# Optimization experiments

Hardware: AMD Instinct MI355X
Metric: run time of the kernel (lower is better)

Reference implementation:

```python
import jax, jax.numpy as jnp
import numpy as np

BINS = 5
POINTS = 2
EPS_DIV = 1e-6
GN_GROUPS = 32
GN_EPS = 1e-5


def bilinear_sum(img, ys, xs):
    """Sum of bilinear samples with zero padding outside the image.
    img: (B, C, H, W); ys, xs: (B, K, H, W) absolute sample coords.
    Returns (B, C, H, W) = sum over K of bilinear(img, ys_k, xs_k)."""
    B, C, H, W = img.shape
    K = ys.shape[1]
    y0 = jnp.floor(ys)
    x0 = jnp.floor(xs)
    imgf = img.reshape(B, C, H * W)
    acc = jnp.zeros((B, C, K, H, W), img.dtype)
    for dy, dx in ((0, 0), (0, 1), (1, 0), (1, 1)):
        yi = y0 + dy
        xi = x0 + dx
        w = (1.0 - jnp.abs(ys - yi)) * (1.0 - jnp.abs(xs - xi))
        valid = (yi >= 0) & (yi <= H - 1) & (xi >= 0) & (xi <= W - 1)
        yc = jnp.clip(yi, 0, H - 1).astype(jnp.int32)
        xc = jnp.clip(xi, 0, W - 1).astype(jnp.int32)
        idx = (yc * W + xc).reshape(B, 1, K * H * W)
        g = jnp.take_along_axis(imgf, idx, axis=2).reshape(B, C, K, H, W)
        acc = acc + (w * valid.astype(img.dtype))[:, None] * g
    return acc.sum(axis=2)


def setup_inputs():
    key = jax.random.key(0)
    ks = jax.random.split(key, 6)
    B, C, H, W = 2, 256, 100, 152
    P, K = POINTS, BINS
    x = jax.random.normal(ks[0], (B, C, H, W), jnp.float32)
    offsets = jax.random.normal(ks[1], (B, P * K * 2, H, W), jnp.float32) * 2.0
    ef_w = jax.random.normal(ks[2], (P * C, C), jnp.float32) * 0.02
    ef_b = jnp.zeros((P * C,), jnp.float32)
    hm1_w = jax.random.normal(ks[3], (P, C, C), jnp.float32) * 0.02
    hm1_b = jnp.zeros((P, C), jnp.float32)
    hm2_w = jax.random.normal(ks[4], (P, C), jnp.float32) * 0.02
    hm2_b = jnp.zeros((P,), jnp.float32)
    merge_w = jax.random.normal(ks[5], (C, P * C), jnp.float32) * 0.02
    merge_b = jnp.zeros((C,), jnp.float32)
    gn_g = jnp.ones((C,), jnp.float32)
    gn_b = jnp.zeros((C,), jnp.float32)
    return {"x": x, "offsets": offsets, "ef_w": ef_w, "ef_b": ef_b,
            "hm1_w": hm1_w, "hm1_b": hm1_b, "hm2_w": hm2_w, "hm2_b": hm2_b,
            "merge_w": merge_w, "merge_b": merge_b, "gn_g": gn_g, "gn_b": gn_b}


def reference(x, offsets, ef_w, ef_b, hm1_w, hm1_b, hm2_w, hm2_b, merge_w, merge_b, gn_g, gn_b):
    B, C, H, W = x.shape
    P, K = POINTS, BINS
    # expand_feat: 1x1 conv C -> P*C
    ef = jnp.einsum('bchw,dc->bdhw', x, ef_w) + ef_b[None, :, None, None]
    efp = ef.reshape(B, P, C, H, W)
    # heatmap: grouped 1x1 conv (per-point) -> ReLU -> grouped 1x1 conv -> exp
    h = jax.nn.relu(jnp.einsum('bpchw,pdc->bpdhw', efp, hm1_w) + hm1_b[None, :, :, None, None])
    heat = jnp.exp(jnp.einsum('bpdhw,pd->bphw', h, hm2_w) + hm2_b[None, :, None, None])  # (B,P,H,W)
    # offsets: (B, P, K, 2, H, W) with channel layout [y, x] per bin.
    # base_offset cancels the [1,bins] kernel grid, so the deform conv with
    # all-ones weights is simply: sum over bins of bilinear samples at
    # (h + off_y, w + off_x).
    off = offsets.reshape(B, P, K, 2, H, W)
    hg = jnp.arange(H, dtype=x.dtype)[None, None, None, :, None]
    wg = jnp.arange(W, dtype=x.dtype)[None, None, None, None, :]
    ys = hg + off[:, :, :, 0]  # (B,P,K,H,W)
    xs = wg + off[:, :, :, 1]
    outs = []
    for p in range(P):
        # sample feat*heat (C channels) and heat (1 channel) together
        img = jnp.concatenate([efp[:, p] * heat[:, p][:, None], heat[:, p][:, None]], axis=1)
        s = bilinear_sum(img, ys[:, p], xs[:, p])  # (B, C+1, H, W)
        outs.append(s[:, :C] / (s[:, C:] + EPS_DIV))
    outs = jnp.concatenate(outs, axis=1)  # (B, P*C, H, W)
    merged = jnp.einsum('bchw,dc->bdhw', outs, merge_w) + merge_b[None, :, None, None]
    # GroupNorm(32, C) + ReLU
    g = merged.reshape(B, GN_GROUPS, C // GN_GROUPS, H, W)
    mu = g.mean(axis=(2, 3, 4), keepdims=True)
    var = g.var(axis=(2, 3, 4), keepdims=True)
    gn = ((g - mu) / jnp.sqrt(var + GN_EPS)).reshape(B, C, H, W)
    gn = gn * gn_g[None, :, None, None] + gn_b[None, :, None, None]
    return jax.nn.relu(gn)
```

## Files before the change

### kernel.cpp

```cpp
#include <hip/hip_runtime.h>

#define BINS 5
#define PTS  2
constexpr int Bx = 2, Cc = 256, Hh = 100, Ww = 152;
constexpr int HW = Hh * Ww;
constexpr int NTILE = 238;
constexpr float EPS_DIV = 1e-6f;
constexpr float GN_EPS  = 1e-5f;

typedef __attribute__((ext_vector_type(8))) short bfrag;
typedef __attribute__((ext_vector_type(4))) float f32x4;

__device__ __forceinline__ ushort f2bf(float f) {
    union { float f; unsigned u; } v; v.f = f;
    unsigned r = v.u + 0x7fffu + ((v.u >> 16) & 1u);
    return (ushort)(r >> 16);
}
__device__ __forceinline__ float bflo(unsigned u) {
    return __uint_as_float(u << 16);
}
__device__ __forceinline__ float bfhi(unsigned u) {
    return __uint_as_float(u & 0xffff0000u);
}
__device__ __forceinline__ unsigned pack2(float a, float b) {
    return (unsigned)f2bf(a) | ((unsigned)f2bf(b) << 16);
}

__global__ __launch_bounds__(256)
void k_wconv(const float* __restrict__ efw, const float* __restrict__ w1,
             const float* __restrict__ mw, ushort* __restrict__ wb)
{
    int gid = blockIdx.x * 256 + threadIdx.x;
    int e = gid * 4;
    int arr = e >> 17, off = e & 131071;
    const float* src = arr == 0 ? efw : (arr == 1 ? w1 : mw);
    float4 v = *(const float4*)(src + off);
    ushort4 o = { f2bf(v.x), f2bf(v.y), f2bf(v.z), f2bf(v.w) };
    *(ushort4*)(wb + e) = o;
}

__global__ __launch_bounds__(256)
void k_xt(const float* __restrict__ x, ushort* __restrict__ xbt)
{
    __shared__ float tile[32][33];
    const int t = threadIdx.x;
    const int hw0 = blockIdx.x * 32;
    const int c0 = blockIdx.y * 32;
    const int b = blockIdx.z;
    const float* xb = x + ((size_t)b * Cc + c0) * HW + hw0;
    const int tx = t & 31, ty = t >> 5;
    #pragma unroll
    for (int r = 0; r < 4; r++) {
        int c = ty + r * 8;
        tile[c][tx] = xb[(size_t)c * HW + tx];
    }
    __syncthreads();
    const int hwl = t >> 3, c4 = (t & 7) * 4;
    ushort4 o = { f2bf(tile[c4 + 0][hwl]), f2bf(tile[c4 + 1][hwl]),
                  f2bf(tile[c4 + 2][hwl]), f2bf(tile[c4 + 3][hwl]) };
    *(ushort4*)&xbt[((size_t)b * HW + hw0 + hwl) * Cc + c0 + c4] = o;
}

__global__ __launch_bounds__(256)
void k_ef(const ushort* __restrict__ xbt, const ushort* __restrict__ wbe,
          const float* __restrict__ efb, ushort* __restrict__ efp)
{
    __shared__ ushort As[128 * 72];
    __shared__ ushort Bs[64 * 72];
    const int t = threadIdx.x;
    const int wv = t >> 6, ln = t & 63;
    const int quad = ln >> 4, l16 = ln & 15;
    const int pix0 = blockIdx.x * 64;
    const int n0 = blockIdx.y * 128;
    const int b = blockIdx.z;
    const ushort* xb = xbt + (size_t)b * HW * Cc;

    f32x4 acc[2][4];
    #pragma unroll
    for (int i = 0; i < 2; i++)
        #pragma unroll
        for (int j = 0; j < 4; j++) acc[i][j] = (f32x4){0.f, 0.f, 0.f, 0.f};

    const int arow = t >> 3, acol = (t & 7) * 8;
    const int srow = t >> 3, scol = (t & 7) * 8;

    for (int k0 = 0; k0 < 256; k0 += 64) {
        #pragma unroll
        for (int r = 0; r < 4; r++) {
            int row = arow + r * 32;
            *(uint4*)&As[row * 72 + acol] =
                *(const uint4*)&wbe[(size_t)(n0 + row) * 256 + k0 + acol];
        }
        #pragma unroll
        for (int r = 0; r < 2; r++) {
            int row = srow + r * 32;
            int pq = pix0 + row; if (pq > HW - 1) pq = HW - 1;
            *(uint4*)&Bs[row * 72 + scol] =
                *(const uint4*)&xb[(size_t)pq * Cc + k0 + scol];
        }
        __syncthreads();
        #pragma unroll
        for (int kk = 0; kk < 64; kk += 32) {
            bfrag af[2], bfr[4];
            #pragma unroll
            for (int dt = 0; dt < 2; dt++)
                af[dt] = *(const bfrag*)&As[(wv * 32 + dt * 16 + l16) * 72 + kk + quad * 8];
            #pragma unroll
            for (int pt = 0; pt < 4; pt++)
                bfr[pt] = *(const bfrag*)&Bs[(pt * 16 + l16) * 72 + kk + quad * 8];
            #pragma unroll
            for (int dt = 0; dt < 2; dt++)
                #pragma unroll
                for (int pt = 0; pt < 4; pt++)
                    acc[dt][pt] = __builtin_amdgcn_mfma_f32_16x16x32_bf16(
                        af[dt], bfr[pt], acc[dt][pt], 0, 0, 0);
        }
        __syncthreads();
    }

    float bias[2][4];
    #pragma unroll
    for (int dt = 0; dt < 2; dt++)
        #pragma unroll
        for (int r = 0; r < 4; r++)
            bias[dt][r] = efb[n0 + wv * 32 + dt * 16 + quad * 4 + r];
    #pragma unroll
    for (int dt = 0; dt < 2; dt++)
        #pragma unroll
        for (int pt = 0; pt < 4; pt++) {
            int pix = pt * 16 + l16;
            int ch = wv * 32 + dt * 16 + quad * 4;
            ushort4 o = { f2bf(acc[dt][pt][0] + bias[dt][0]),
                          f2bf(acc[dt][pt][1] + bias[dt][1]),
                          f2bf(acc[dt][pt][2] + bias[dt][2]),
                          f2bf(acc[dt][pt][3] + bias[dt][3]) };
            *(ushort4*)&As[pix * 136 + ch] = o;
        }
    __syncthreads();
    const int p = n0 >> 8, cbase = n0 & 255;
    ushort* outb = efp + (size_t)((b * PTS + p) * HW) * Cc;
    #pragma unroll
    for (int r = 0; r < 4; r++) {
        int pix = (t >> 4) + r * 16;
        int ch8 = (t & 15) * 8;
        if (pix0 + pix < HW)
            *(uint4*)&outb[(size_t)(pix0 + pix) * Cc + cbase + ch8] =
                *(const uint4*)&As[pix * 136 + ch8];
    }
}

__global__ __launch_bounds__(256)
void k_heat(const ushort* __restrict__ efp, const ushort* __restrict__ wb1,
            const float* __restrict__ b1, const float* __restrict__ w2,
            const float* __restrict__ b2, float* __restrict__ heat)
{
    __shared__ ushort As[256 * 72];
    __shared__ ushort Bs[64 * 72];
    __shared__ float red[4][64];
    const int t = threadIdx.x;
    const int wv = t >> 6, ln = t & 63;
    const int quad = ln >> 4, l16 = ln & 15;
    const int pix0 = blockIdx.x * 64;
    const int p = blockIdx.y;
    const int b = blockIdx.z;
    const ushort* efb_ = efp + (size_t)((b * PTS + p) * HW) * Cc;
    const ushort* w1p = wb1 + (size_t)p * Cc * Cc;

    f32x4 acc[4][4];
    #pragma unroll
    for (int i = 0; i < 4; i++)
        #pragma unroll
        for (int j = 0; j < 4; j++) acc[i][j] = (f32x4){0.f, 0.f, 0.f, 0.f};

    const int srow = t >> 3, scol = (t & 7) * 8;

    for (int k0 = 0; k0 < 256; k0 += 64) {
        #pragma unroll
        for (int r = 0; r < 8; r++) {
            int row = srow + r * 32;
            *(uint4*)&As[row * 72 + scol] =
                *(const uint4*)&w1p[(size_t)row * 256 + k0 + scol];
        }
        #pragma unroll
        for (int r = 0; r < 2; r++) {
            int row = srow + r * 32;
            int pq = pix0 + row; if (pq > HW - 1) pq = HW - 1;
            *(uint4*)&Bs[row * 72 + scol] =
                *(const uint4*)&efb_[(size_t)pq * Cc + k0 + scol];
        }
        __syncthreads();
        #pragma unroll
        for (int kk = 0; kk < 64; kk += 32) {
            bfrag af[4], bfr[4];
            #pragma unroll
            for (int dt = 0; dt < 4; dt++)
                af[dt] = *(const bfrag*)&As[(wv * 64 + dt * 16 + l16) * 72 + kk + quad * 8];
            #pragma unroll
            for (int pt = 0; pt < 4; pt++)
                bfr[pt] = *(const bfrag*)&Bs[(pt * 16 + l16) * 72 + kk + quad * 8];
            #pragma unroll
            for (int dt = 0; dt < 4; dt++)
                #pragma unroll
                for (int pt = 0; pt < 4; pt++)
                    acc[dt][pt] = __builtin_amdgcn_mfma_f32_16x16x32_bf16(
                        af[dt], bfr[pt], acc[dt][pt], 0, 0, 0);
        }
        __syncthreads();
    }

    const float* b1p = b1 + p * 256;
    const float* w2p = w2 + p * 256;
    float s[4] = {0.f, 0.f, 0.f, 0.f};
    #pragma unroll
    for (int dt = 0; dt < 4; dt++) {
        int chb = wv * 64 + dt * 16 + quad * 4;
        float bb[4], ww[4];
        #pragma unroll
        for (int r = 0; r < 4; r++) { bb[r] = b1p[chb + r]; ww[r] = w2p[chb + r]; }
        #pragma unroll
        for (int pt = 0; pt < 4; pt++)
            #pragma unroll
            for (int r = 0; r < 4; r++) {
                float h = acc[dt][pt][r] + bb[r];
                h = h > 0.f ? h : 0.f;
                s[pt] += ww[r] * h;
            }
    }
    #pragma unroll
    for (int pt = 0; pt < 4; pt++) {
        s[pt] += __shfl_xor(s[pt], 16);
        s[pt] += __shfl_xor(s[pt], 32);
    }
    if (ln < 16) {
        #pragma unroll
        for (int pt = 0; pt < 4; pt++) red[wv][pt * 16 + ln] = s[pt];
    }
    __syncthreads();
    if (t < 64) {
        float v = red[0][t] + red[1][t] + red[2][t] + red[3][t] + b2[p];
        int m = pix0 + t;
        if (m < HW) heat[(size_t)(b * PTS + p) * HW + m] = expf(v);
    }
}

__global__ __launch_bounds__(256)
void k_sample(const ushort* __restrict__ efp, const float* __restrict__ heat,
              const float* __restrict__ offs, ushort* __restrict__ outs)
{
    __shared__ uint2 s_wo[32][20];
    const int t = threadIdx.x;
    const int bid = blockIdx.x;
    const int nx = (bid & 7) * 60 + (bid >> 3);
    if (nx >= 475) return;
    const int m0 = nx * 32;
    const int p = blockIdx.y;
    const int b = blockIdx.z;
    const float* heat_bp = heat + (size_t)(b * PTS + p) * HW;

    if (t < 32 * BINS) {
        int j = t / BINS, k = t % BINS;
        int hw = m0 + j;
        int hh = hw / Ww, ww = hw % Ww;
        int chy = (p * BINS + k) * 2;
        float oy = offs[((size_t)b * (PTS * BINS * 2) + chy)     * HW + hw];
        float ox = offs[((size_t)b * (PTS * BINS * 2) + chy + 1) * HW + hw];
        float ysf = (float)hh + oy;
        float xsf = (float)ww + ox;
        float y0 = floorf(ysf), x0 = floorf(xsf);
        #pragma unroll
        for (int dy = 0; dy < 2; dy++)
            #pragma unroll
            for (int dx = 0; dx < 2; dx++) {
                float yi = y0 + dy, xi = x0 + dx;
                float wgt = (1.f - fabsf(ysf - yi)) * (1.f - fabsf(xsf - xi));
                bool valid = (yi >= 0.f) && (yi <= (float)(Hh - 1)) &&
                             (xi >= 0.f) && (xi <= (float)(Ww - 1));
                int yc = (int)yi; yc = yc < 0 ? 0 : (yc > Hh - 1 ? Hh - 1 : yc);
                int xc = (int)xi; xc = xc < 0 ? 0 : (xc > Ww - 1 ? Ww - 1 : xc);
                int idx = yc * Ww + xc;
                float wh = valid ? wgt * heat_bp[idx] : 0.f;
                s_wo[j][k * 4 + dy * 2 + dx] =
                    make_uint2(__float_as_uint(wh), (unsigned)idx << 9);
            }
    }
    __syncthreads();
    if (t < 32) {
        float s = 0.f;
        #pragma unroll
        for (int u = 0; u < 20; u++) s += __uint_as_float(s_wo[t][u].x);
        float inv = 1.f / (s + EPS_DIV);
        #pragma unroll
        for (int u = 0; u < 20; u++)
            s_wo[t][u].x = __float_as_uint(__uint_as_float(s_wo[t][u].x) * inv);
    }
    __syncthreads();

    const int wv = t >> 6, ln = t & 63;
    const int half = ln >> 5, c8 = ln & 31;
    const char* efbase = (const char*)(efp + (size_t)((b * PTS + p) * HW) * Cc)
                         + c8 * 16;
    ushort* ob = outs + ((size_t)(b * HW + m0)) * (PTS * Cc) + p * Cc + c8 * 8;
    #pragma unroll
    for (int i = 0; i < 8; i += 2) {
        const int j = wv * 8 + i + half;
        float a[8] = {0.f, 0.f, 0.f, 0.f, 0.f, 0.f, 0.f, 0.f};
        #pragma unroll
        for (int u = 0; u < 20; u++) {
            uint2 wo = s_wo[j][u];
            uint4 v = *(const uint4*)(efbase + wo.y);
            float w = __uint_as_float(wo.x);
            a[0] += w * bflo(v.x); a[1] += w * bfhi(v.x);
            a[2] += w * bflo(v.y); a[3] += w * bfhi(v.y);
            a[4] += w * bflo(v.z); a[5] += w * bfhi(v.z);
            a[6] += w * bflo(v.w); a[7] += w * bfhi(v.w);
        }
        uint4 o = { pack2(a[0], a[1]), pack2(a[2], a[3]),
                    pack2(a[4], a[5]), pack2(a[6], a[7]) };
        *(uint4*)(ob + (size_t)j * (PTS * Cc)) = o;
    }
}

__global__ __launch_bounds__(256)
void k_merge(const ushort* __restrict__ outs, const ushort* __restrict__ wbm,
             const float* __restrict__ mb, ushort* __restrict__ mgb,
             float* __restrict__ part2)
{
    __shared__ ushort As[64 * 72];
    __shared__ ushort Bs[64 * 72];
    const int t = threadIdx.x;
    const int wv = t >> 6, ln = t & 63;
    const int quad = ln >> 4, l16 = ln & 15;
    const int pix0 = blockIdx.x * 64;
    const int n0 = blockIdx.y * 64;
    const int b = blockIdx.z;
    const ushort* ob = outs + (size_t)b * HW * (PTS * Cc);

    f32x4 acc[4];
    #pragma unroll
    for (int j = 0; j < 4; j++) acc[j] = (f32x4){0.f, 0.f, 0.f, 0.f};

    const int srow = t >> 3, scol = (t & 7) * 8;

    for (int k0 = 0; k0 < 512; k0 += 64) {
        #pragma unroll
        for (int r = 0; r < 2; r++) {
            int row = srow + r * 32;
            *(uint4*)&As[row * 72 + scol] =
                *(const uint4*)&wbm[(size_t)(n0 + row) * 512 + k0 + scol];
        }
        #pragma unroll
        for (int r = 0; r < 2; r++) {
            int row = srow + r * 32;
            int pq = pix0 + row; if (pq > HW - 1) pq = HW - 1;
            *(uint4*)&Bs[row * 72 + scol] =
                *(const uint4*)&ob[(size_t)pq * (PTS * Cc) + k0 + scol];
        }
        __syncthreads();
        #pragma unroll
        for (int kk = 0; kk < 64; kk += 32) {
            bfrag af = *(const bfrag*)&As[(wv * 16 + l16) * 72 + kk + quad * 8];
            #pragma unroll
            for (int pt = 0; pt < 4; pt++) {
                bfrag bfr = *(const bfrag*)&Bs[(pt * 16 + l16) * 72 + kk + quad * 8];
                acc[pt] = __builtin_amdgcn_mfma_f32_16x16x32_bf16(
                    af, bfr, acc[pt], 0, 0, 0);
            }
        }
        __syncthreads();
    }

    const int ch = n0 + wv * 16 + quad * 4;
    float bias[4];
    #pragma unroll
    for (int r = 0; r < 4; r++) bias[r] = mb[ch + r];

    float sacc = 0.f, qacc = 0.f;
    #pragma unroll
    for (int pt = 0; pt < 4; pt++) {
        int pix = pix0 + pt * 16 + l16;
        if (pix < HW) {
            #pragma unroll
            for (int r = 0; r < 4; r++) {
                float v = acc[pt][r] + bias[r];
                mgb[((size_t)b * Cc + ch + r) * HW + pix] = f2bf(v);
                sacc += v; qacc += v * v;
            }
        }
    }
    #pragma unroll
    for (int off = 1; off <= 16; off <<= 1) {
        sacc += __shfl_xor(sacc, off);
        qacc += __shfl_xor(qacc, off);
    }
    if ((ln & 31) == 0) {
        int g = (n0 >> 3) + wv * 2 + (quad >> 1);
        size_t idx = ((size_t)(b * 32 + g) * NTILE + blockIdx.x) * 2;
        part2[idx + 0] = sacc;
        part2[idx + 1] = qacc;
    }
}

__global__ __launch_bounds__(256)
void k_gnfinal(const float* __restrict__ part2, float* __restrict__ statf)
{
    const int bg = blockIdx.x;
    const int t = threadIdx.x;
    float s = 0.f, q = 0.f;
    if (t < NTILE) {
        s = part2[((size_t)bg * NTILE + t) * 2 + 0];
        q = part2[((size_t)bg * NTILE + t) * 2 + 1];
    }
    #pragma unroll
    for (int off = 1; off <= 32; off <<= 1) {
        s += __shfl_xor(s, off);
        q += __shfl_xor(q, off);
    }
    __shared__ float rs[4], rq[4];
    int wid = t >> 6;
    if ((t & 63) == 0) { rs[wid] = s; rq[wid] = q; }
    __syncthreads();
    if (t == 0) {
        float S = rs[0] + rs[1] + rs[2] + rs[3];
        float Q = rq[0] + rq[1] + rq[2] + rq[3];
        const float n = 8.f * HW;
        float mean = S / n;
        float var  = Q / n - mean * mean;
        statf[bg * 2 + 0] = mean;
        statf[bg * 2 + 1] = rsqrtf(var + GN_EPS);
    }
}

__global__ __launch_bounds__(256)
void k_gnapply(const ushort* __restrict__ mgb, const float* __restrict__ statf,
               const float* __restrict__ gg, const float* __restrict__ gb,
               float* __restrict__ out)
{
    const int i8 = blockIdx.x * 256 + threadIdx.x;
    const int i = i8 * 8;
    const int CHW = Cc * HW;
    const int b = i / CHW;
    const int r = i - b * CHW;
    const int c = r / HW;
    const int g = c >> 3;
    float mean = statf[(b * 32 + g) * 2 + 0];
    float istd = statf[(b * 32 + g) * 2 + 1];
    float sc = istd * gg[c];
    float sh = gb[c] - mean * sc;
    uint4 v = *(const uint4*)(mgb + i);
    float4 o0, o1;
    o0.x = fmaxf(bflo(v.x) * sc + sh, 0.f);
    o0.y = fmaxf(bfhi(v.x) * sc + sh, 0.f);
    o0.z = fmaxf(bflo(v.y) * sc + sh, 0.f);
    o0.w = fmaxf(bfhi(v.y) * sc + sh, 0.f);
    o1.x = fmaxf(bflo(v.z) * sc + sh, 0.f);
    o1.y = fmaxf(bfhi(v.z) * sc + sh, 0.f);
    o1.z = fmaxf(bflo(v.w) * sc + sh, 0.f);
    o1.w = fmaxf(bfhi(v.w) * sc + sh, 0.f);
    *(float4*)(out + i)     = o0;
    *(float4*)(out + i + 4) = o1;
}

extern "C" void kernel_launch(void* const* d_in, const int* in_sizes, int n_in,
                              void* d_out, int out_size, void* d_ws, size_t ws_size,
                              hipStream_t stream)
{
    const float* x    = (const float*)d_in[0];
    const float* offs = (const float*)d_in[1];
    const float* efw  = (const float*)d_in[2];
    const float* efb  = (const float*)d_in[3];
    const float* w1   = (const float*)d_in[4];
    const float* b1   = (const float*)d_in[5];
    const float* w2   = (const float*)d_in[6];
    const float* b2   = (const float*)d_in[7];
    const float* mw   = (const float*)d_in[8];
    const float* mb   = (const float*)d_in[9];
    const float* gg   = (const float*)d_in[10];
    const float* gb   = (const float*)d_in[11];
    float* out = (float*)d_out;

    ushort* wb    = (ushort*)d_ws;
    ushort* wbe   = wb;
    ushort* wb1   = wb + 131072;
    ushort* wbm   = wb + 262144;
    ushort* efp   = wb + 393216;
    ushort* outsb = efp + (size_t)Bx * PTS * HW * Cc;
    ushort* xbt   = outsb + (size_t)Bx * HW * PTS * Cc;
    ushort* mgb   = xbt + (size_t)Bx * HW * Cc;
    float*  heat  = (float*)(mgb + (size_t)Bx * Cc * HW);
    float*  part2 = heat + (size_t)Bx * PTS * HW;
    float*  statf = part2 + (size_t)64 * NTILE * 2;

    dim3 blk(256);
    k_wconv  <<<dim3(384),              blk, 0, stream>>>(efw, w1, mw, wb);
    k_xt     <<<dim3(475, 8, Bx),       blk, 0, stream>>>(x, xbt);
    k_ef     <<<dim3(238, 4, Bx),       blk, 0, stream>>>(xbt, wbe, efb, efp);
    k_heat   <<<dim3(238, PTS, Bx),     blk, 0, stream>>>(efp, wb1, b1, w2, b2, heat);
    k_sample <<<dim3(480, PTS, Bx),     blk, 0, stream>>>(efp, heat, offs, outsb);
    k_merge  <<<dim3(NTILE, 4, Bx),     blk, 0, stream>>>(outsb, wbm, mb, mgb, part2);
    k_gnfinal<<<dim3(64),               blk, 0, stream>>>(part2, statf);
    k_gnapply<<<dim3(Bx * Cc * HW / 8 / 256), blk, 0, stream>>>(mgb, statf, gg, gb, out);
}
```

Baseline: 212.3 us.

## Fold expand-conv weights into heat and merge GEMMs, sample raw x directly

Uses the linearity of the 1x1 expand conv to remove the k_ef GEMM and the efp intermediate. The expand weights are pre-multiplied into the heat-MLP first layer and into the merge weights, and bilinear sampling now reads the transposed bf16 x. The expand bias is carried as a per-pixel term: the normalized heat-weight sum is saved to sbuf and multiplied by a folded bias vector in the merge epilogue. This drops a large GEMM and its memory traffic, but adds a small fp32 weight-combination kernel each call and changes bf16 rounding points.

```diff
diff --git a/kernel.cpp b/kernel.cpp
--- a/kernel.cpp
+++ b/kernel.cpp
@@ -27,19 +27,6 @@
 }
 
 __global__ __launch_bounds__(256)
-void k_wconv(const float* __restrict__ efw, const float* __restrict__ w1,
-             const float* __restrict__ mw, ushort* __restrict__ wb)
-{
-    int gid = blockIdx.x * 256 + threadIdx.x;
-    int e = gid * 4;
-    int arr = e >> 17, off = e & 131071;
-    const float* src = arr == 0 ? efw : (arr == 1 ? w1 : mw);
-    float4 v = *(const float4*)(src + off);
-    ushort4 o = { f2bf(v.x), f2bf(v.y), f2bf(v.z), f2bf(v.w) };
-    *(ushort4*)(wb + e) = o;
-}
-
-__global__ __launch_bounds__(256)
 void k_xt(const float* __restrict__ x, ushort* __restrict__ xbt)
 {
     __shared__ float tile[32][33];
@@ -62,34 +49,96 @@
 }
 
 __global__ __launch_bounds__(256)
-void k_ef(const ushort* __restrict__ xbt, const ushort* __restrict__ wbe,
-          const float* __restrict__ efb, ushort* __restrict__ efp)
-{
-    __shared__ ushort As[128 * 72];
+void k_wcomb(const float* __restrict__ efw, const float* __restrict__ w1,
+             const float* __restrict__ mw, ushort* __restrict__ whb,
+             ushort* __restrict__ cmb)
+{
+    __shared__ float Wt[16][256];
+    const int t = threadIdx.x;
+    const int tile = blockIdx.x, p = blockIdx.y, which = blockIdx.z;
+    if (which == 0) {
+        const float* src = w1 + (size_t)p * 65536 + (size_t)tile * 16 * 256;
+        #pragma unroll
+        for (int i = 0; i < 16; i++) Wt[i][t] = src[i * 256 + t];
+    } else {
+        #pragma unroll
+        for (int i = 0; i < 16; i++)
+            Wt[i][t] = mw[((size_t)(tile * 16 + i)) * 512 + p * 256 + t];
+    }
+    __syncthreads();
+    float acc[16];
+    #pragma unroll
+    for (int r = 0; r < 16; r++) acc[r] = 0.f;
+    const float* eb = efw + (size_t)p * 256 * 256;
+    for (int d = 0; d < 256; d++) {
+        float v = eb[(size_t)d * 256 + t];
+        #pragma unroll
+        for (int r = 0; r < 16; r++) acc[r] += Wt[r][d] * v;
+    }
+    if (which == 0) {
+        #pragma unroll
+        for (int r = 0; r < 16; r++)
+            whb[(size_t)p * 65536 + (size_t)(tile * 16 + r) * 256 + t] = f2bf(acc[r]);
+    } else {
+        #pragma unroll
+        for (int r = 0; r < 16; r++)
+            cmb[(size_t)(tile * 16 + r) * 512 + p * 256 + t] = f2bf(acc[r]);
+    }
+}
+
+__global__ __launch_bounds__(256)
+void k_vbias(const float* __restrict__ efb, const float* __restrict__ w1,
+             const float* __restrict__ b1, const float* __restrict__ mw,
+             float* __restrict__ hbias, float* __restrict__ vb)
+{
+    __shared__ float eb[256];
+    const int t = threadIdx.x;
+    const int which = blockIdx.x >> 1, p = blockIdx.x & 1;
+    eb[t] = efb[p * 256 + t];
+    __syncthreads();
+    float a = 0.f;
+    if (which == 0) {
+        const float* row = w1 + ((size_t)p * 256 + t) * 256;
+        for (int d = 0; d < 256; d++) a += row[d] * eb[d];
+        hbias[p * 256 + t] = a + b1[p * 256 + t];
+    } else {
+        const float* row = mw + (size_t)t * 512 + p * 256;
+        for (int d = 0; d < 256; d++) a += row[d] * eb[d];
+        vb[p * 256 + t] = a;
+    }
+}
+
+__global__ __launch_bounds__(256)
+void k_heat(const ushort* __restrict__ xbt, const ushort* __restrict__ whb,
+            const float* __restrict__ hbias, const float* __restrict__ w2,
+            const float* __restrict__ b2, float* __restrict__ heat)
+{
+    __shared__ ushort As[256 * 72];
     __shared__ ushort Bs[64 * 72];
+    __shared__ float red[4][64];
     const int t = threadIdx.x;
     const int wv = t >> 6, ln = t & 63;
     const int quad = ln >> 4, l16 = ln & 15;
     const int pix0 = blockIdx.x * 64;
-    const int n0 = blockIdx.y * 128;
+    const int p = blockIdx.y;
     const int b = blockIdx.z;
     const ushort* xb = xbt + (size_t)b * HW * Cc;
-
-    f32x4 acc[2][4];
-    #pragma unroll
-    for (int i = 0; i < 2; i++)
+    const ushort* w1p = whb + (size_t)p * Cc * Cc;
+
+    f32x4 acc[4][4];
+    #pragma unroll
+    for (int i = 0; i < 4; i++)
         #pragma unroll
         for (int j = 0; j < 4; j++) acc[i][j] = (f32x4){0.f, 0.f, 0.f, 0.f};
 
-    const int arow = t >> 3, acol = (t & 7) * 8;
     const int srow = t >> 3, scol = (t & 7) * 8;
 
     for (int k0 = 0; k0 < 256; k0 += 64) {
         #pragma unroll
-        for (int r = 0; r < 4; r++) {
-            int row = arow + r * 32;
-            *(uint4*)&As[row * 72 + acol] =
-                *(const uint4*)&wbe[(size_t)(n0 + row) * 256 + k0 + acol];
+        for (int r = 0; r < 8; r++) {
+            int row = srow + r * 32;
+            *(uint4*)&As[row * 72 + scol] =
+                *(const uint4*)&w1p[(size_t)row * 256 + k0 + scol];
         }
         #pragma unroll
         for (int r = 0; r < 2; r++) {
@@ -101,96 +150,6 @@
         __syncthreads();
         #pragma unroll
         for (int kk = 0; kk < 64; kk += 32) {
-            bfrag af[2], bfr[4];
-            #pragma unroll
-            for (int dt = 0; dt < 2; dt++)
-                af[dt] = *(const bfrag*)&As[(wv * 32 + dt * 16 + l16) * 72 + kk + quad * 8];
-            #pragma unroll
-            for (int pt = 0; pt < 4; pt++)
-                bfr[pt] = *(const bfrag*)&Bs[(pt * 16 + l16) * 72 + kk + quad * 8];
-            #pragma unroll
-            for (int dt = 0; dt < 2; dt++)
-                #pragma unroll
-                for (int pt = 0; pt < 4; pt++)
-                    acc[dt][pt] = __builtin_amdgcn_mfma_f32_16x16x32_bf16(
-                        af[dt], bfr[pt], acc[dt][pt], 0, 0, 0);
-        }
-        __syncthreads();
-    }
-
-    float bias[2][4];
-    #pragma unroll
-    for (int dt = 0; dt < 2; dt++)
-        #pragma unroll
-        for (int r = 0; r < 4; r++)
-            bias[dt][r] = efb[n0 + wv * 32 + dt * 16 + quad * 4 + r];
-    #pragma unroll
-    for (int dt = 0; dt < 2; dt++)
-        #pragma unroll
-        for (int pt = 0; pt < 4; pt++) {
-            int pix = pt * 16 + l16;
-            int ch = wv * 32 + dt * 16 + quad * 4;
-            ushort4 o = { f2bf(acc[dt][pt][0] + bias[dt][0]),
-                          f2bf(acc[dt][pt][1] + bias[dt][1]),
-                          f2bf(acc[dt][pt][2] + bias[dt][2]),
-                          f2bf(acc[dt][pt][3] + bias[dt][3]) };
-            *(ushort4*)&As[pix * 136 + ch] = o;
-        }
-    __syncthreads();
-    const int p = n0 >> 8, cbase = n0 & 255;
-    ushort* outb = efp + (size_t)((b * PTS + p) * HW) * Cc;
-    #pragma unroll
-    for (int r = 0; r < 4; r++) {
-        int pix = (t >> 4) + r * 16;
-        int ch8 = (t & 15) * 8;
-        if (pix0 + pix < HW)
-            *(uint4*)&outb[(size_t)(pix0 + pix) * Cc + cbase + ch8] =
-                *(const uint4*)&As[pix * 136 + ch8];
-    }
-}
-
-__global__ __launch_bounds__(256)
-void k_heat(const ushort* __restrict__ efp, const ushort* __restrict__ wb1,
-            const float* __restrict__ b1, const float* __restrict__ w2,
-            const float* __restrict__ b2, float* __restrict__ heat)
-{
-    __shared__ ushort As[256 * 72];
-    __shared__ ushort Bs[64 * 72];
-    __shared__ float red[4][64];
-    const int t = threadIdx.x;
-    const int wv = t >> 6, ln = t & 63;
-    const int quad = ln >> 4, l16 = ln & 15;
-    const int pix0 = blockIdx.x * 64;
-    const int p = blockIdx.y;
-    const int b = blockIdx.z;
-    const ushort* efb_ = efp + (size_t)((b * PTS + p) * HW) * Cc;
-    const ushort* w1p = wb1 + (size_t)p * Cc * Cc;
-
-    f32x4 acc[4][4];
-    #pragma unroll
-    for (int i = 0; i < 4; i++)
-        #pragma unroll
-        for (int j = 0; j < 4; j++) acc[i][j] = (f32x4){0.f, 0.f, 0.f, 0.f};
-
-    const int srow = t >> 3, scol = (t & 7) * 8;
-
-    for (int k0 = 0; k0 < 256; k0 += 64) {
-        #pragma unroll
-        for (int r = 0; r < 8; r++) {
-            int row = srow + r * 32;
-            *(uint4*)&As[row * 72 + scol] =
-                *(const uint4*)&w1p[(size_t)row * 256 + k0 + scol];
-        }
-        #pragma unroll
-        for (int r = 0; r < 2; r++) {
-            int row = srow + r * 32;
-            int pq = pix0 + row; if (pq > HW - 1) pq = HW - 1;
-            *(uint4*)&Bs[row * 72 + scol] =
-                *(const uint4*)&efb_[(size_t)pq * Cc + k0 + scol];
-        }
-        __syncthreads();
-        #pragma unroll
-        for (int kk = 0; kk < 64; kk += 32) {
             bfrag af[4], bfr[4];
             #pragma unroll
             for (int dt = 0; dt < 4; dt++)
@@ -208,7 +167,7 @@
         __syncthreads();
     }
 
-    const float* b1p = b1 + p * 256;
+    const float* b1p = hbias + p * 256;
     const float* w2p = w2 + p * 256;
     float s[4] = {0.f, 0.f, 0.f, 0.f};
     #pragma unroll
@@ -244,8 +203,9 @@
 }
 
 __global__ __launch_bounds__(256)
-void k_sample(const ushort* __restrict__ efp, const float* __restrict__ heat,
-              const float* __restrict__ offs, ushort* __restrict__ outs)
+void k_sample(const ushort* __restrict__ xbt, const float* __restrict__ heat,
+              const float* __restrict__ offs, ushort* __restrict__ outs,
+              float* __restrict__ sbuf)
 {
     __shared__ uint2 s_wo[32][20];
     const int t = threadIdx.x;
@@ -292,13 +252,13 @@
         #pragma unroll
         for (int u = 0; u < 20; u++)
             s_wo[t][u].x = __float_as_uint(__uint_as_float(s_wo[t][u].x) * inv);
+        sbuf[(size_t)(b * PTS + p) * HW + m0 + t] = s * inv;
     }
     __syncthreads();
 
     const int wv = t >> 6, ln = t & 63;
     const int half = ln >> 5, c8 = ln & 31;
-    const char* efbase = (const char*)(efp + (size_t)((b * PTS + p) * HW) * Cc)
-                         + c8 * 16;
+    const char* efbase = (const char*)(xbt + (size_t)b * HW * Cc) + c8 * 16;
     ushort* ob = outs + ((size_t)(b * HW + m0)) * (PTS * Cc) + p * Cc + c8 * 8;
     #pragma unroll
     for (int i = 0; i < 8; i += 2) {
@@ -321,8 +281,9 @@
 }
 
 __global__ __launch_bounds__(256)
-void k_merge(const ushort* __restrict__ outs, const ushort* __restrict__ wbm,
-             const float* __restrict__ mb, ushort* __restrict__ mgb,
+void k_merge(const ushort* __restrict__ outs, const ushort* __restrict__ cmb,
+             const float* __restrict__ mb, const float* __restrict__ vb,
+             const float* __restrict__ sbuf, ushort* __restrict__ mgb,
              float* __restrict__ part2)
 {
     __shared__ ushort As[64 * 72];
@@ -346,7 +307,7 @@
         for (int r = 0; r < 2; r++) {
             int row = srow + r * 32;
             *(uint4*)&As[row * 72 + scol] =
-                *(const uint4*)&wbm[(size_t)(n0 + row) * 512 + k0 + scol];
+                *(const uint4*)&cmb[(size_t)(n0 + row) * 512 + k0 + scol];
         }
         #pragma unroll
         for (int r = 0; r < 2; r++) {
@@ -370,18 +331,25 @@
     }
 
     const int ch = n0 + wv * 16 + quad * 4;
-    float bias[4];
-    #pragma unroll
-    for (int r = 0; r < 4; r++) bias[r] = mb[ch + r];
+    float bias[4], v0[4], v1[4];
+    #pragma unroll
+    for (int r = 0; r < 4; r++) {
+        bias[r] = mb[ch + r];
+        v0[r] = vb[ch + r];
+        v1[r] = vb[256 + ch + r];
+    }
+    const float* s0p = sbuf + (size_t)(b * PTS + 0) * HW;
+    const float* s1p = sbuf + (size_t)(b * PTS + 1) * HW;
 
     float sacc = 0.f, qacc = 0.f;
     #pragma unroll
     for (int pt = 0; pt < 4; pt++) {
         int pix = pix0 + pt * 16 + l16;
         if (pix < HW) {
+            float s0 = s0p[pix], s1 = s1p[pix];
             #pragma unroll
             for (int r = 0; r < 4; r++) {
-                float v = acc[pt][r] + bias[r];
+                float v = acc[pt][r] + bias[r] + v0[r] * s0 + v1[r] * s1;
                 mgb[((size_t)b * Cc + ch + r) * HW + pix] = f2bf(v);
                 sacc += v; qacc += v * v;
             }
@@ -478,25 +446,25 @@
     const float* gb   = (const float*)d_in[11];
     float* out = (float*)d_out;
 
-    ushort* wb    = (ushort*)d_ws;
-    ushort* wbe   = wb;
-    ushort* wb1   = wb + 131072;
-    ushort* wbm   = wb + 262144;
-    ushort* efp   = wb + 393216;
-    ushort* outsb = efp + (size_t)Bx * PTS * HW * Cc;
-    ushort* xbt   = outsb + (size_t)Bx * HW * PTS * Cc;
-    ushort* mgb   = xbt + (size_t)Bx * HW * Cc;
+    ushort* whb   = (ushort*)d_ws;
+    ushort* cmb   = whb + 131072;
+    ushort* xbt   = cmb + 131072;
+    ushort* outsb = xbt + (size_t)Bx * HW * Cc;
+    ushort* mgb   = outsb + (size_t)Bx * HW * PTS * Cc;
     float*  heat  = (float*)(mgb + (size_t)Bx * Cc * HW);
-    float*  part2 = heat + (size_t)Bx * PTS * HW;
+    float*  sbuf  = heat + (size_t)Bx * PTS * HW;
+    float*  hbias = sbuf + (size_t)Bx * PTS * HW;
+    float*  vb    = hbias + 512;
+    float*  part2 = vb + 512;
     float*  statf = part2 + (size_t)64 * NTILE * 2;
 
     dim3 blk(256);
-    k_wconv  <<<dim3(384),              blk, 0, stream>>>(efw, w1, mw, wb);
-    k_xt     <<<dim3(475, 8, Bx),       blk, 0, stream>>>(x, xbt);
-    k_ef     <<<dim3(238, 4, Bx),       blk, 0, stream>>>(xbt, wbe, efb, efp);
-    k_heat   <<<dim3(238, PTS, Bx),     blk, 0, stream>>>(efp, wb1, b1, w2, b2, heat);
-    k_sample <<<dim3(480, PTS, Bx),     blk, 0, stream>>>(efp, heat, offs, outsb);
-    k_merge  <<<dim3(NTILE, 4, Bx),     blk, 0, stream>>>(outsb, wbm, mb, mgb, part2);
-    k_gnfinal<<<dim3(64),               blk, 0, stream>>>(part2, statf);
+    k_xt     <<<dim3(475, 8, Bx),   blk, 0, stream>>>(x, xbt);
+    k_wcomb  <<<dim3(16, 2, 2),     blk, 0, stream>>>(efw, w1, mw, whb, cmb);
+    k_vbias  <<<dim3(4),            blk, 0, stream>>>(efb, w1, b1, mw, hbias, vb);
+    k_heat   <<<dim3(238, PTS, Bx), blk, 0, stream>>>(xbt, whb, hbias, w2, b2, heat);
+    k_sample <<<dim3(480, PTS, Bx), blk, 0, stream>>>(xbt, heat, offs, outsb, sbuf);
+    k_merge  <<<dim3(NTILE, 4, Bx), blk, 0, stream>>>(outsb, cmb, mb, vb, sbuf, mgb, part2);
+    k_gnfinal<<<dim3(64),           blk, 0, stream>>>(part2, statf);
     k_gnapply<<<dim3(Bx * Cc * HW / 8 / 256), blk, 0, stream>>>(mgb, statf, gg, gb, out);
 }
```

New measurement: 215.4 us. About the same (+1.5%).
